# Optimization experiments

Measured on AMD Instinct MI355X. Metric: run time of the kernel, lower is better.

The kernel has to match this reference:

```python
import jax, jax.numpy as jnp
import numpy as np

H = 512          # hidden_size == input_size
K = 32768        # number of child cell inputs (lattice merge fan-in)


def setup_inputs() -> dict:
    key = jax.random.key(0)
    ks = jax.random.split(key, 8)
    s = 1.0 / np.sqrt(H)  # keep matmul outputs O(1)
    return {
        "input_": jax.random.normal(ks[0], (1, H), dtype=jnp.float32),
        "c_input": jax.random.normal(ks[1], (K, H), dtype=jnp.float32),
        "h_0": jax.random.normal(ks[2], (1, H), dtype=jnp.float32),
        "c_0": jax.random.normal(ks[3], (1, H), dtype=jnp.float32),
        "weight_ih": jax.random.normal(ks[4], (H, 3 * H), dtype=jnp.float32) * s,
        "weight_hh": jax.random.normal(ks[5], (H, 3 * H), dtype=jnp.float32) * s,
        "bias": jnp.zeros((3 * H,), dtype=jnp.float32),
        "alpha_weight_ih": jax.random.normal(ks[6], (H, H), dtype=jnp.float32) * s,
        "alpha_weight_hh": jax.random.normal(ks[7], (H, H), dtype=jnp.float32) * s,
    }


def reference(input_, c_input, h_0, c_0, weight_ih, weight_hh, bias,
              alpha_weight_ih, alpha_weight_hh):
    # Gate pre-activations: addmm(bias, h_0, W_hh) + input_ @ W_ih  -> [1, 3H]
    gates = h_0 @ weight_hh + bias + input_ @ weight_ih
    i, o, g = jnp.split(gates, 3, axis=1)        # each [1, H]
    i = jax.nn.sigmoid(i)
    o = jax.nn.sigmoid(o)
    g = jnp.tanh(g)

    # Variable-child softmax-weighted cell merge (non-empty c_input branch)
    alpha_wi = input_ @ alpha_weight_ih          # [1, H], broadcast over K
    alpha_wh = c_input @ alpha_weight_hh         # [K, H]
    alpha = jax.nn.sigmoid(alpha_wi + alpha_wh)  # [K, H]

    logits = jnp.concatenate([i, alpha], axis=0)  # [K+1, H]
    w = jnp.exp(logits)
    w = w / (w.sum(axis=0, keepdims=True) + 1e-12)

    merge = jnp.concatenate([g, c_input], axis=0)  # [K+1, H]
    c_1 = (merge * w).sum(axis=0, keepdims=True)   # [1, H]
    h_1 = o * jnp.tanh(c_1)                        # [1, H]
    return h_1, c_1
```

## Files before the change

### kernel.cpp

```cpp
#include <hip/hip_runtime.h>
#include <hip/hip_bf16.h>
#include <stdint.h>

#define Hdim 512
#define KC   32768

typedef __hip_bfloat16 bf16;
typedef __attribute__((ext_vector_type(8))) short short8;
typedef __attribute__((ext_vector_type(4))) float float4v;
typedef __attribute__((ext_vector_type(4))) unsigned int uint4v;

__device__ __forceinline__ unsigned int pack_bf16_trunc(float e0, float e1) {
  union { float f; unsigned int u; } a, b;
  a.f = e0; b.f = e1;
  return __builtin_amdgcn_perm(b.u, a.u, 0x07060302u);
}

__global__ __launch_bounds__(1024) void prep_wt_kernel(
    const float* __restrict__ input_, const float* __restrict__ h_0,
    const float* __restrict__ w_ih, const float* __restrict__ w_hh,
    const float* __restrict__ a_w_ih, const float* __restrict__ a_w_hh,
    float* __restrict__ gates, float* __restrict__ awi, bf16* __restrict__ wt) {
  const int t = threadIdx.x;
  if (blockIdx.x < 8) {
    __shared__ float h0s[Hdim], ins[Hdim];
    __shared__ float red[4][256];
    const int js = t & 255, ds = t >> 8;
    for (int i = t; i < Hdim; i += 1024) { h0s[i] = h_0[i]; ins[i] = input_[i]; }
    __syncthreads();
    const int j = blockIdx.x * 256 + js;
    float acc = 0.f;
    if (j < 1536) {
#pragma unroll 8
      for (int d = ds * 128; d < ds * 128 + 128; ++d)
        acc += h0s[d] * w_hh[(size_t)d * 1536 + j] + ins[d] * w_ih[(size_t)d * 1536 + j];
    } else {
      const int jj = j - 1536;
#pragma unroll 8
      for (int d = ds * 128; d < ds * 128 + 128; ++d)
        acc += ins[d] * a_w_ih[(size_t)d * Hdim + jj];
    }
    red[ds][js] = acc;
    __syncthreads();
    if (t < 256) {
      const int jo = blockIdx.x * 256 + t;
      float s = red[0][t] + red[1][t] + red[2][t] + red[3][t];
      if (jo < 1536) gates[jo] = s;
      else           awi[jo - 1536] = s;
    }
  } else {
    __shared__ float tile[64][65];
    const int b = blockIdx.x - 8;
    const int d0 = (b & 7) * 64, h0 = (b >> 3) * 64;
    const int tx = t & 63, tw = t >> 6;
#pragma unroll
    for (int r = 0; r < 4; ++r) {
      const int row = r * 16 + tw;
      tile[row][tx] = a_w_hh[(size_t)(d0 + row) * Hdim + h0 + tx];
    }
    __syncthreads();
#pragma unroll
    for (int r = 0; r < 4; ++r) {
      const int row = r * 16 + tw;
      wt[(size_t)(h0 + row) * Hdim + d0 + tx] = __float2bfloat16(tile[tx][row]);
    }
  }
}

__global__ __launch_bounds__(256) void gemm_reduce_kernel(
    const float* __restrict__ c_input, const bf16* __restrict__ WT,
    const float* __restrict__ awi,
    float* __restrict__ pw, float* __restrict__ pwc) {
  __shared__ __align__(16) bf16 As[128 * 64];
  __shared__ __align__(16) bf16 Bs[128 * 64];
  __shared__ float red_w[2][128];
  __shared__ float red_wc[2][128];

  const int tid  = threadIdx.x;
  const int lane = tid & 63;
  const int wv   = tid >> 6;
  const int wm   = wv & 1;
  const int wn   = wv >> 1;
  const int lm   = lane & 15;
  const int lq   = lane >> 4;

  const int id     = blockIdx.x;
  const int kk_idx = ((id >> 5) << 3) | (id & 7);
  const int h_idx  = (id >> 3) & 3;
  const int kk0 = kk_idx * 128;
  const int h0  = h_idx * 128;

  const int ar_base = tid >> 3;
  const int acol    = (tid & 7) * 8;
  const int aga     = tid & 7;
  const int br_base = wv * 8 + (lane >> 3);
  const int bg      = (lane & 7) ^ (lane >> 3);
  const int bcol    = (lane & 7) * 8;

  float4v acc[4][4];
#pragma unroll
  for (int i = 0; i < 4; ++i)
#pragma unroll
    for (int j = 0; j < 4; ++j)
      acc[i][j] = (float4v){0.f, 0.f, 0.f, 0.f};

  char* AsB = (char*)As;
  char* BsB = (char*)Bs;

  float4v pa0[4], pa1[4];
  short8  pb[4];
#pragma unroll
  for (int j = 0; j < 4; ++j) {
    const float* p = c_input + (size_t)(kk0 + j * 32 + ar_base) * Hdim + acol;
    pa0[j] = *(const float4v*)p;
    pa1[j] = *(const float4v*)(p + 4);
  }
#pragma unroll
  for (int r = 0; r < 4; ++r)
    pb[r] = *(const short8*)(WT + (size_t)(h0 + r * 32 + br_base) * Hdim + bcol);

#pragma unroll 1
  for (int it = 0; it < 8; ++it) {
    __syncthreads();
#pragma unroll
    for (int j = 0; j < 4; ++j) {
      const int row = j * 32 + ar_base;
      uint4v u;
      u[0] = pack_bf16_trunc(pa0[j][0], pa0[j][1]);
      u[1] = pack_bf16_trunc(pa0[j][2], pa0[j][3]);
      u[2] = pack_bf16_trunc(pa1[j][0], pa1[j][1]);
      u[3] = pack_bf16_trunc(pa1[j][2], pa1[j][3]);
      *(uint4v*)(AsB + row * 128 + ((aga ^ (row & 7)) * 16)) = u;
    }
#pragma unroll
    for (int r = 0; r < 4; ++r) {
      const int row = r * 32 + br_base;
      *(short8*)(BsB + row * 128 + bg * 16) = pb[r];
    }
    __syncthreads();
    if (it < 7) {
      const int d0 = (it + 1) * 64;
#pragma unroll
      for (int j = 0; j < 4; ++j) {
        const float* p = c_input + (size_t)(kk0 + j * 32 + ar_base) * Hdim + d0 + acol;
        pa0[j] = *(const float4v*)p;
        pa1[j] = *(const float4v*)(p + 4);
      }
#pragma unroll
      for (int r = 0; r < 4; ++r)
        pb[r] = *(const short8*)(WT + (size_t)(h0 + r * 32 + br_base) * Hdim + d0 + bcol);
    }
#pragma unroll
    for (int ks = 0; ks < 2; ++ks) {
      short8 a[4], b[4];
#pragma unroll
      for (int mt = 0; mt < 4; ++mt) {
        const int row = wm * 64 + mt * 16 + lm;
        a[mt] = *(const short8*)(AsB + row * 128 + (((ks * 4 + lq) ^ (lm & 7)) * 16));
      }
#pragma unroll
      for (int nt = 0; nt < 4; ++nt) {
        const int row = wn * 64 + nt * 16 + lm;
        b[nt] = *(const short8*)(BsB + row * 128 + (((ks * 4 + lq) ^ (lm & 7)) * 16));
      }
#pragma unroll
      for (int mt = 0; mt < 4; ++mt)
#pragma unroll
        for (int nt = 0; nt < 4; ++nt)
          acc[mt][nt] = __builtin_amdgcn_mfma_f32_16x16x32_bf16(a[mt], b[nt], acc[mt][nt], 0, 0, 0);
    }
  }

  float awi_l[4];
#pragma unroll
  for (int nt = 0; nt < 4; ++nt)
    awi_l[nt] = awi[h0 + wn * 64 + nt * 16 + lm];

  float sw[4] = {0.f, 0.f, 0.f, 0.f}, swc[4] = {0.f, 0.f, 0.f, 0.f};
#pragma unroll
  for (int nt = 0; nt < 4; ++nt) {
    const int h = h0 + wn * 64 + nt * 16 + lm;
#pragma unroll
    for (int mt = 0; mt < 4; ++mt) {
      const int kkb = kk0 + wm * 64 + mt * 16 + lq * 4;
#pragma unroll
      for (int r = 0; r < 4; ++r) {
        float v = acc[mt][nt][r] + awi_l[nt];
        float alpha = 1.f / (1.f + __expf(-v));
        float e = __expf(alpha);
        float c = c_input[(size_t)(kkb + r) * Hdim + h];
        sw[nt]  += e;
        swc[nt] += e * c;
      }
    }
  }
#pragma unroll
  for (int nt = 0; nt < 4; ++nt) {
    sw[nt]  += __shfl_xor(sw[nt], 16, 64);
    sw[nt]  += __shfl_xor(sw[nt], 32, 64);
    swc[nt] += __shfl_xor(swc[nt], 16, 64);
    swc[nt] += __shfl_xor(swc[nt], 32, 64);
  }
  if (lq == 0) {
#pragma unroll
    for (int nt = 0; nt < 4; ++nt) {
      red_w[wm][wn * 64 + nt * 16 + lm]  = sw[nt];
      red_wc[wm][wn * 64 + nt * 16 + lm] = swc[nt];
    }
  }
  __syncthreads();
  if (tid < 128) {
    pw[(size_t)kk_idx * Hdim + h0 + tid]  = red_w[0][tid] + red_w[1][tid];
    pwc[(size_t)kk_idx * Hdim + h0 + tid] = red_wc[0][tid] + red_wc[1][tid];
  }
}

__global__ __launch_bounds__(1024) void finalize_kernel(
    const float* __restrict__ pw, const float* __restrict__ pwc,
    const float* __restrict__ gates, const float* __restrict__ bias,
    float* __restrict__ out) {
  __shared__ float rsw[16][64], rswc[16][64];
  const int t = threadIdx.x;
  const int hl = t & 63, q = t >> 6;
  const int hh = blockIdx.x * 64 + hl;
  float sw = 0.f, swc = 0.f;
#pragma unroll 8
  for (int kb = q * 16; kb < q * 16 + 16; ++kb) {
    sw  += pw[(size_t)kb * Hdim + hh];
    swc += pwc[(size_t)kb * Hdim + hh];
  }
  rsw[q][hl] = sw; rswc[q][hl] = swc;
  __syncthreads();
  if (t < 64) {
    const int h = blockIdx.x * 64 + t;
    sw = 0.f; swc = 0.f;
#pragma unroll
    for (int qq = 0; qq < 16; ++qq) { sw += rsw[qq][t]; swc += rswc[qq][t]; }
    float ipre = gates[h] + bias[h];
    float opre = gates[Hdim + h] + bias[Hdim + h];
    float gpre = gates[2 * Hdim + h] + bias[2 * Hdim + h];
    float ei = expf(1.f / (1.f + expf(-ipre)));
    float g  = tanhf(gpre);
    float o  = 1.f / (1.f + expf(-opre));
    float denom = ei + sw + 1e-12f;
    float c1 = (ei * g + swc) / denom;
    float h1 = o * tanhf(c1);
    out[h]        = h1;
    out[Hdim + h] = c1;
  }
}

extern "C" void kernel_launch(void* const* d_in, const int* in_sizes, int n_in,
                              void* d_out, int out_size, void* d_ws, size_t ws_size,
                              hipStream_t stream) {
  const float* input_  = (const float*)d_in[0];
  const float* c_input = (const float*)d_in[1];
  const float* h_0     = (const float*)d_in[2];
  const float* w_ih    = (const float*)d_in[4];
  const float* w_hh    = (const float*)d_in[5];
  const float* bias    = (const float*)d_in[6];
  const float* a_w_ih  = (const float*)d_in[7];
  const float* a_w_hh  = (const float*)d_in[8];

  char* ws = (char*)d_ws;
  float* pw    = (float*)ws;
  float* pwc   = (float*)(ws + 512 * 1024);
  float* gates = (float*)(ws + 1024 * 1024);
  float* awi   = (float*)(ws + 1024 * 1024 + 6144);
  bf16*  WT    = (bf16*)(ws + 1024 * 1024 + 8192);

  hipLaunchKernelGGL(prep_wt_kernel, dim3(72), dim3(1024), 0, stream,
                     input_, h_0, w_ih, w_hh, a_w_ih, a_w_hh, gates, awi, WT);
  hipLaunchKernelGGL(gemm_reduce_kernel, dim3(1024), dim3(256), 0, stream,
                     c_input, WT, awi, pw, pwc);
  hipLaunchKernelGGL(finalize_kernel, dim3(8), dim3(1024), 0, stream,
                     pw, pwc, gates, bias, (float*)d_out);
}
```

Before: 154.1 us.

## Load A fragments directly from global memory into MFMA registers, drop A LDS staging

The GEMM kernel no longer stages the c_input tile through shared memory. Each lane now reads its MFMA A-fragment straight from global fp32 memory and converts it to bf16 in registers. This removes the LDS writes and reads for A and halves shared memory use, which may allow more blocks per CU. In exchange, global reads are no longer prefetched a stage ahead, so their latency sits on the MFMA critical path. Both wn waves also read the same A rows, which relies on the cache to avoid duplicate traffic.

New measurement: 198.0 us. 28.5% more time.

```diff
diff --git a/kernel.cpp b/kernel.cpp
--- a/kernel.cpp
+++ b/kernel.cpp
@@ -8,7 +8,6 @@
 typedef __hip_bfloat16 bf16;
 typedef __attribute__((ext_vector_type(8))) short short8;
 typedef __attribute__((ext_vector_type(4))) float float4v;
-typedef __attribute__((ext_vector_type(4))) unsigned int uint4v;
 
 __device__ __forceinline__ unsigned int pack_bf16_trunc(float e0, float e1) {
   union { float f; unsigned int u; } a, b;
@@ -71,7 +70,6 @@
     const float* __restrict__ c_input, const bf16* __restrict__ WT,
     const float* __restrict__ awi,
     float* __restrict__ pw, float* __restrict__ pwc) {
-  __shared__ __align__(16) bf16 As[128 * 64];
   __shared__ __align__(16) bf16 Bs[128 * 64];
   __shared__ float red_w[2][128];
   __shared__ float red_wc[2][128];
@@ -90,9 +88,6 @@
   const int kk0 = kk_idx * 128;
   const int h0  = h_idx * 128;
 
-  const int ar_base = tid >> 3;
-  const int acol    = (tid & 7) * 8;
-  const int aga     = tid & 7;
   const int br_base = wv * 8 + (lane >> 3);
   const int bg      = (lane & 7) ^ (lane >> 3);
   const int bcol    = (lane & 7) * 8;
@@ -104,34 +99,19 @@
     for (int j = 0; j < 4; ++j)
       acc[i][j] = (float4v){0.f, 0.f, 0.f, 0.f};
 
-  char* AsB = (char*)As;
   char* BsB = (char*)Bs;
 
-  float4v pa0[4], pa1[4];
-  short8  pb[4];
-#pragma unroll
-  for (int j = 0; j < 4; ++j) {
-    const float* p = c_input + (size_t)(kk0 + j * 32 + ar_base) * Hdim + acol;
-    pa0[j] = *(const float4v*)p;
-    pa1[j] = *(const float4v*)(p + 4);
-  }
+  const float* arow = c_input + (size_t)(kk0 + wm * 64 + lm) * Hdim;
+
+  short8 pb[4];
 #pragma unroll
   for (int r = 0; r < 4; ++r)
     pb[r] = *(const short8*)(WT + (size_t)(h0 + r * 32 + br_base) * Hdim + bcol);
 
 #pragma unroll 1
   for (int it = 0; it < 8; ++it) {
-    __syncthreads();
-#pragma unroll
-    for (int j = 0; j < 4; ++j) {
-      const int row = j * 32 + ar_base;
-      uint4v u;
-      u[0] = pack_bf16_trunc(pa0[j][0], pa0[j][1]);
-      u[1] = pack_bf16_trunc(pa0[j][2], pa0[j][3]);
-      u[2] = pack_bf16_trunc(pa1[j][0], pa1[j][1]);
-      u[3] = pack_bf16_trunc(pa1[j][2], pa1[j][3]);
-      *(uint4v*)(AsB + row * 128 + ((aga ^ (row & 7)) * 16)) = u;
-    }
+    const int d0 = it * 64;
+    __syncthreads();
 #pragma unroll
     for (int r = 0; r < 4; ++r) {
       const int row = r * 32 + br_base;
@@ -139,25 +119,26 @@
     }
     __syncthreads();
     if (it < 7) {
-      const int d0 = (it + 1) * 64;
-#pragma unroll
-      for (int j = 0; j < 4; ++j) {
-        const float* p = c_input + (size_t)(kk0 + j * 32 + ar_base) * Hdim + d0 + acol;
-        pa0[j] = *(const float4v*)p;
-        pa1[j] = *(const float4v*)(p + 4);
+#pragma unroll
+      for (int r = 0; r < 4; ++r)
+        pb[r] = *(const short8*)(WT + (size_t)(h0 + r * 32 + br_base) * Hdim + d0 + 64 + bcol);
+    }
+#pragma unroll
+    for (int ks = 0; ks < 2; ++ks) {
+      short8 a[4];
+#pragma unroll
+      for (int mt = 0; mt < 4; ++mt) {
+        const float* p = arow + (size_t)(mt * 16) * Hdim + d0 + ks * 32 + lq * 8;
+        float4v a0 = *(const float4v*)p;
+        float4v a1 = *(const float4v*)(p + 4);
+        union { unsigned int u[4]; short8 s; } af;
+        af.u[0] = pack_bf16_trunc(a0[0], a0[1]);
+        af.u[1] = pack_bf16_trunc(a0[2], a0[3]);
+        af.u[2] = pack_bf16_trunc(a1[0], a1[1]);
+        af.u[3] = pack_bf16_trunc(a1[2], a1[3]);
+        a[mt] = af.s;
       }
-#pragma unroll
-      for (int r = 0; r < 4; ++r)
-        pb[r] = *(const short8*)(WT + (size_t)(h0 + r * 32 + br_base) * Hdim + d0 + bcol);
-    }
-#pragma unroll
-    for (int ks = 0; ks < 2; ++ks) {
-      short8 a[4], b[4];
-#pragma unroll
-      for (int mt = 0; mt < 4; ++mt) {
-        const int row = wm * 64 + mt * 16 + lm;
-        a[mt] = *(const short8*)(AsB + row * 128 + (((ks * 4 + lq) ^ (lm & 7)) * 16));
-      }
+      short8 b[4];
 #pragma unroll
       for (int nt = 0; nt < 4; ++nt) {
         const int row = wn * 64 + nt * 16 + lm;
```
